# Optimization experiments

Hardware: AMD Instinct MI355X
Metric: run time of the kernel (lower is better)

## Reference

```python
import jax, jax.numpy as jnp
import numpy as np

D_MODEL = 512
D_STATE = 64
N_LAYERS = 6
L_SEQ = 784
BATCH = 64


def _layernorm(x, g, b, eps=1e-5):
    mu = x.mean(-1, keepdims=True)
    var = ((x - mu) ** 2).mean(-1, keepdims=True)
    return (x - mu) * jax.lax.rsqrt(var + eps) * g + b


def _s4d_kernel(log_dt, log_A_real, A_imag, C_re, C_im, L):
    # log_dt: (H,), others: (H, N). Returns real conv kernel (H, L).
    dt = jnp.exp(log_dt)[:, None]                      # (H,1)
    A = -jnp.exp(log_A_real) + 1j * A_imag             # (H,N) complex
    C = C_re + 1j * C_im                               # (H,N)
    dtA = A * dt                                       # (H,N)
    Cd = C * (jnp.exp(dtA) - 1.0) / A                  # ZOH-discretized C
    # Vandermonde: V[h,n,l] = exp(dtA[h,n] * l)
    V = jnp.exp(dtA[:, :, None] * jnp.arange(L, dtype=jnp.float32))  # (H,N,L)
    K = 2.0 * jnp.einsum('hn,hnl->hl', Cd, V).real     # (H,L)
    return K


def _s4_fftconv(u, K, D):
    # u: (B,L,H), K: (H,L), D: (H,)
    L = u.shape[1]
    uf = jnp.fft.rfft(u, 2 * L, axis=1)                # (B, L+1, H)
    kf = jnp.fft.rfft(K.T, 2 * L, axis=0)              # (L+1, H)
    y = jnp.fft.irfft(uf * kf[None], 2 * L, axis=1)[:, :L]
    return y + u * D


def setup_inputs() -> dict:
    key = jax.random.key(0)
    ks = jax.random.split(key, 12)
    H, N, NL = D_MODEL, D_STATE, N_LAYERS
    x = jax.random.normal(ks[0], (BATCH, L_SEQ, 1), dtype=jnp.float32)
    enc_w = jax.random.normal(ks[1], (1, H), dtype=jnp.float32) * 0.5
    enc_b = jnp.zeros((H,), dtype=jnp.float32)
    # S4D-Lin style init, stacked over layers
    log_dt = jnp.tile(
        jax.random.uniform(ks[2], (H,), minval=np.log(0.001), maxval=np.log(0.1)),
        (NL, 1))                                        # (NL,H)
    log_A_real = jnp.full((NL, H, N), jnp.log(0.5), dtype=jnp.float32)
    A_imag = jnp.tile(np.pi * jnp.arange(N, dtype=jnp.float32), (NL, H, 1))
    C_re = jax.random.normal(ks[3], (NL, H, N), dtype=jnp.float32) * (0.5 ** 0.5)
    C_im = jax.random.normal(ks[4], (NL, H, N), dtype=jnp.float32) * (0.5 ** 0.5)
    D = jax.random.normal(ks[5], (NL, H), dtype=jnp.float32)
    ln_g = jnp.ones((NL, H), dtype=jnp.float32)
    ln_b = jnp.zeros((NL, H), dtype=jnp.float32)
    fn_g = jnp.ones((H,), dtype=jnp.float32)
    fn_b = jnp.zeros((H,), dtype=jnp.float32)
    dec_w = jax.random.normal(ks[6], (H, 10), dtype=jnp.float32) / jnp.sqrt(H)
    dec_b = jnp.zeros((10,), dtype=jnp.float32)
    return dict(x=x, enc_w=enc_w, enc_b=enc_b, log_dt=log_dt,
                log_A_real=log_A_real, A_imag=A_imag, C_re=C_re, C_im=C_im,
                D=D, ln_g=ln_g, ln_b=ln_b, fn_g=fn_g, fn_b=fn_b,
                dec_w=dec_w, dec_b=dec_b)


def reference(x, enc_w, enc_b, log_dt, log_A_real, A_imag, C_re, C_im, D,
              ln_g, ln_b, fn_g, fn_b, dec_w, dec_b):
    h = x @ enc_w + enc_b                               # (B,L,H)
    L = h.shape[1]
    for i in range(log_dt.shape[0]):                    # fixed n_layers
        K = _s4d_kernel(log_dt[i], log_A_real[i], A_imag[i], C_re[i], C_im[i], L)
        z = _s4_fftconv(h, K, D[i])                     # S4 output (dropout=eval)
        h = _layernorm(h + z, ln_g[i], ln_b[i])         # residual + LN
    h = _layernorm(h, fn_g, fn_b)
    h = h.mean(axis=1)                                  # mean pool over seq
    return h @ dec_w + dec_b                            # (B,10)
```

## Files before the change

### kernel.cpp

```cpp
#include <hip/hip_runtime.h>
#include <hip/hip_bf16.h>

#define HD 512
#define NST 64
#define NLAY 6
#define LSEQ 784
#define BB 64
#define NKA 848
#define TOFF 800
#define LPADROWS 800
#define KSTR 850
#define CHK2 5
#define NCH 5
#define UTS2 9

typedef unsigned short u16;
typedef short s8v __attribute__((ext_vector_type(8)));
typedef float f16v __attribute__((ext_vector_type(16)));
typedef u16  u4h __attribute__((ext_vector_type(4)));
typedef u16  u8h __attribute__((ext_vector_type(8)));

__device__ __forceinline__ unsigned f2b(float f)
{
    unsigned u = __builtin_bit_cast(unsigned, f);
    return (u + 0x7FFFu + ((u >> 16) & 1u)) >> 16;
}
__device__ __forceinline__ float b2f16(u16 v)
{
    unsigned u = ((unsigned)v) << 16;
    return __builtin_bit_cast(float, u);
}

__global__ void precompute_k(const float* __restrict__ log_dt,
                             const float* __restrict__ log_A_real,
                             const float* __restrict__ A_imag,
                             const float* __restrict__ C_re,
                             const float* __restrict__ C_im,
                             float* __restrict__ lamr, float* __restrict__ lami,
                             float* __restrict__ dtr,  float* __restrict__ dti,
                             float* __restrict__ c2r,  float* __restrict__ c2i)
{
    int t = blockIdx.x * 256 + threadIdx.x;
    if (t >= NLAY * HD * NST) return;
    int ih = t >> 6;
    float dt  = expf(log_dt[ih]);
    float are = -expf(log_A_real[t]);
    float aim = A_imag[t];
    float dr = are * dt, di = aim * dt;
    float er = expf(dr);
    float sn, cs; __sincosf(di, &sn, &cs);
    float lr = er * cs, li = er * sn;
    float e1r = lr - 1.0f, e1i = li;
    float den = are * are + aim * aim;
    float qr = (e1r * are + e1i * aim) / den;
    float qi = (e1i * are - e1r * aim) / den;
    float crv = C_re[t], civ = C_im[t];
    lamr[t] = lr; lami[t] = li; dtr[t] = dr; dti[t] = di;
    c2r[t] = 2.0f * (crv * qr - civ * qi);
    c2i[t] = 2.0f * (crv * qi + civ * qr);
}

__global__ void kq_k(const float* __restrict__ lamr, const float* __restrict__ lami,
                     const float* __restrict__ dtr,  const float* __restrict__ dti,
                     const float* __restrict__ c2r,  const float* __restrict__ c2i,
                     u16* __restrict__ KA)
{
    int t = blockIdx.x * 256 + threadIdx.x;
    int dc = t % 49;
    int ih = t / 49;
    int d0 = dc * 16;
    float acc[16];
#pragma unroll
    for (int k = 0; k < 16; k++) acc[k] = 0.f;
    int base = ih * 64;
    for (int n = 0; n < 64; n++) {
        float lr = lamr[base + n], li = lami[base + n];
        float dr = dtr[base + n],  di = dti[base + n];
        float cr = c2r[base + n],  ci = c2i[base + n];
        float e = __expf(dr * (float)d0);
        float sn, cs; __sincosf(di * (float)d0, &sn, &cs);
        float pr = e * cs, pi = e * sn;
#pragma unroll
        for (int k = 0; k < 16; k++) {
            acc[k] = fmaf(cr, pr, fmaf(-ci, pi, acc[k]));
            float nr = pr * lr - pi * li;
            pi = fmaf(pr, li, pi * lr);
            pr = nr;
        }
    }
    u16* kap = KA + (size_t)ih * NKA;
#pragma unroll
    for (int k = 0; k < 16; k++)
        kap[TOFF - (d0 + k)] = (u16)f2b(acc[k]);
    if (dc == 0)  for (int z = TOFF + 1; z < NKA; z++) kap[z] = 0;
    if (dc == 48) for (int z = 0; z < TOFF - 783; z++) kap[z] = 0;
}

__global__ void xt_k(const float* __restrict__ x, float* __restrict__ xT)
{
    int t = blockIdx.x * 256 + threadIdx.x;
    int l = t >> 6, b = t & 63;
    xT[t] = x[b * LSEQ + l];
}

__global__ void encoder_k(const float* __restrict__ xT, const float* __restrict__ ew,
                          const float* __restrict__ eb, u16* __restrict__ Vb)
{
    int g = blockIdx.x * 256 + threadIdx.x;
    int bo = g & 7;
    int h  = (g >> 3) & 511;
    int l  = g >> 12;
    const float4* xp = (const float4*)&xT[l * BB + 8 * bo];
    float4 a0 = xp[0], a1 = xp[1];
    float w = ew[h], bb = eb[h];
    unsigned p0 = f2b(fmaf(a0.x, w, bb)) | (f2b(fmaf(a0.y, w, bb)) << 16);
    unsigned p1 = f2b(fmaf(a0.z, w, bb)) | (f2b(fmaf(a0.w, w, bb)) << 16);
    unsigned p2 = f2b(fmaf(a1.x, w, bb)) | (f2b(fmaf(a1.y, w, bb)) << 16);
    unsigned p3 = f2b(fmaf(a1.z, w, bb)) | (f2b(fmaf(a1.w, w, bb)) << 16);
    *(uint4*)&Vb[((size_t)l * HD + h) * BB + 8 * bo] = (uint4){p0, p1, p2, p3};
}

__global__ __launch_bounds__(128, 4)
void conv_k(const u16* __restrict__ Vb, u16* __restrict__ V2,
            const u16* __restrict__ KA, const float* __restrict__ Dvec)
{
    __shared__ __align__(16) u16 KR[6816];
    __shared__ __align__(16) unsigned UT[2][64 * UTS2];

    const int thr = threadIdx.x;
    const int h   = blockIdx.x & 511;
    const int c   = blockIdx.x >> 9;
    const int w   = thr >> 6;
    const int lane = thr & 63;
    const int n2 = lane & 31;
    const int qp = lane >> 5;
    const int JTN = 10 * c + 10;

    const u16* kap = KA + (size_t)h * NKA;
    {
        int s = thr & 7, ch = thr >> 3;
        int i0 = ch * 53;
        int i1 = (i0 + 53 < NKA) ? (i0 + 53) : NKA;
        u16* kr = KR + KSTR * s + ((8 - s) & 7);
        for (int i = i0; i < i1; i++) kr[i] = kap[i];
    }

    const int jj = thr >> 4;
    const int bq = thr & 15;
    {
        const u16* p = &Vb[((size_t)(2 * jj) * HD + h) * BB + 4 * bq];
        u4h r0 = *(const u4h*)p;
        u4h r1 = *(const u4h*)(p + (size_t)HD * BB);
        unsigned* up = &UT[0][0];
#pragma unroll
        for (int i = 0; i < 4; i++)
            up[(4 * bq + i) * UTS2 + jj] = (unsigned)r0[i] | ((unsigned)r1[i] << 16);
    }
    __syncthreads();

    f16v acc[CHK2];
#pragma unroll
    for (int i = 0; i < CHK2; i++)
#pragma unroll
        for (int r = 0; r < 16; r++) acc[i][r] = 0.f;

    const float dcoef = 1.0f + Dvec[h];

    const int s = lane & 7;
    const u16* krb = KR + KSTR * s + ((8 - s) & 7)
                     + (TOFF - 160 * c) + 8 * qp - n2;
    const unsigned* bb0 = &UT[0][(32 * w + n2) * UTS2 + 4 * qp];
    const unsigned* bb1 = &UT[1][(32 * w + n2) * UTS2 + 4 * qp];

    for (int jt = 0; jt < JTN; ++jt) {
        u4h r0, r1;
        const bool more = (jt + 1) < JTN;
        if (more) {
            int j = 16 * (jt + 1) + 2 * jj;
            const u16* p = &Vb[((size_t)j * HD + h) * BB + 4 * bq];
            r0 = *(const u4h*)p;
            r1 = *(const u4h*)(p + (size_t)HD * BB);
        }
        const unsigned* bb = (jt & 1) ? bb1 : bb0;
        union { unsigned u[4]; s8v v; } bu;
        bu.u[0] = bb[0]; bu.u[1] = bb[1]; bu.u[2] = bb[2]; bu.u[3] = bb[3];

        const u16* ap0 = krb + 16 * jt;
#pragma unroll
        for (int lt = 0; lt < CHK2; ++lt) {
            if (jt > 10 * c + 2 * lt + 1) continue;
            s8v av = *(const s8v*)__builtin_assume_aligned(ap0 - 32 * lt, 16);
            acc[lt] = __builtin_amdgcn_mfma_f32_32x32x16_bf16(av, bu.v, acc[lt], 0, 0, 0);
        }
        if (more) {
            unsigned* up = &UT[(jt & 1) ^ 1][0];
#pragma unroll
            for (int i = 0; i < 4; i++)
                up[(4 * bq + i) * UTS2 + jj] = (unsigned)r0[i] | ((unsigned)r1[i] << 16);
        }
        __syncthreads();
    }

#pragma unroll
    for (int lt = 0; lt < CHK2; ++lt) {
        const int l0 = 32 * (5 * c + lt) + 4 * qp;
#pragma unroll
        for (int r = 0; r < 16; ++r) {
            int l = l0 + (r & 3) + 8 * (r >> 2);
            size_t a = ((size_t)l * HD + h) * BB + 32 * w + n2;
            V2[a] = (u16)f2b(fmaf(dcoef, b2f16(Vb[a]), acc[lt][r]));
        }
    }
}

__global__ __launch_bounds__(512)
void lnT_k(const u16* __restrict__ src, u16* __restrict__ dst,
           const float* __restrict__ gp, const float* __restrict__ bp)
{
    __shared__ float redS[64][65], redQ[64][65];
    __shared__ float mus[64], rss[64];
    __shared__ float gs[512], bs[512];
    const int thr = threadIdx.x;
    const int bo = thr & 7;
    const int hg = thr >> 3;
    const size_t l = blockIdx.x;
    gs[thr] = gp[thr]; bs[thr] = bp[thr];

    const u16* sp = &src[(l * HD + hg * 8) * BB + 8 * bo];
    float v[64];
    float s[8] = {0, 0, 0, 0, 0, 0, 0, 0};
    float q[8] = {0, 0, 0, 0, 0, 0, 0, 0};
#pragma unroll
    for (int k = 0; k < 8; k++) {
        u8h r = *(const u8h*)(sp + (size_t)k * BB);
#pragma unroll
        for (int i = 0; i < 8; i++) {
            float x = b2f16(r[i]);
            v[k * 8 + i] = x;
            s[i] += x;
            q[i] = fmaf(x, x, q[i]);
        }
    }
#pragma unroll
    for (int i = 0; i < 8; i++) { redS[hg][8 * bo + i] = s[i]; redQ[hg][8 * bo + i] = q[i]; }
    __syncthreads();
    if (thr < 64) {
        float ts = 0.f, tq = 0.f;
#pragma unroll
        for (int g = 0; g < 64; g++) { ts += redS[g][thr]; tq += redQ[g][thr]; }
        float mu = ts * (1.0f / HD);
        mus[thr] = mu;
        rss[thr] = rsqrtf(tq * (1.0f / HD) - mu * mu + 1e-5f);
    }
    __syncthreads();
    float mu[8], rs[8];
#pragma unroll
    for (int i = 0; i < 8; i++) { mu[i] = mus[8 * bo + i]; rs[i] = rss[8 * bo + i]; }
    u16* dp = &dst[(l * HD + hg * 8) * BB + 8 * bo];
#pragma unroll
    for (int k = 0; k < 8; k++) {
        float g = gs[hg * 8 + k], bb = bs[hg * 8 + k];
        u8h w;
#pragma unroll
        for (int i = 0; i < 8; i++)
            w[i] = (u16)f2b(fmaf((v[k * 8 + i] - mu[i]) * rs[i], g, bb));
        *(u8h*)(dp + (size_t)k * BB) = w;
    }
}

__global__ void pool_k(const u16* __restrict__ Vb, float* __restrict__ PO)
{
    __shared__ float red[4][64];
    int h = blockIdx.x;
    int b = threadIdx.x & 63;
    int lg = threadIdx.x >> 6;
    const u16* p = &Vb[(size_t)h * BB + b];
    float s = 0.f;
    for (int l = lg; l < LSEQ; l += 4) s += b2f16(p[(size_t)l * HD * BB]);
    red[lg][b] = s;
    __syncthreads();
    if (threadIdx.x < 64) {
        float t = red[0][b] + red[1][b] + red[2][b] + red[3][b];
        PO[h * BB + b] = t * (1.0f / LSEQ);
    }
}

__global__ void dec_k(const float* __restrict__ PO, const float* __restrict__ w,
                      const float* __restrict__ bias, float* __restrict__ out)
{
    int t = blockIdx.x * 256 + threadIdx.x;
    if (t >= BB * 10) return;
    int cc = t % 10, b = t / 10;
    float acc = bias[cc];
    for (int hh = 0; hh < HD; hh++)
        acc = fmaf(PO[hh * BB + b], w[hh * 10 + cc], acc);
    out[t] = acc;
}

extern "C" void kernel_launch(void* const* d_in, const int* in_sizes, int n_in,
                              void* d_out, int out_size, void* d_ws, size_t ws_size,
                              hipStream_t stream)
{
    const float* x   = (const float*)d_in[0];
    const float* ew  = (const float*)d_in[1];
    const float* eb  = (const float*)d_in[2];
    const float* ldt = (const float*)d_in[3];
    const float* lar = (const float*)d_in[4];
    const float* aim = (const float*)d_in[5];
    const float* cre = (const float*)d_in[6];
    const float* cim = (const float*)d_in[7];
    const float* Dp  = (const float*)d_in[8];
    const float* lng = (const float*)d_in[9];
    const float* lnb = (const float*)d_in[10];
    const float* fng = (const float*)d_in[11];
    const float* fnb = (const float*)d_in[12];
    const float* dw  = (const float*)d_in[13];
    const float* db  = (const float*)d_in[14];
    float* out = (float*)d_out;

    const size_t SZ  = (size_t)BB * LSEQ * HD;
    const size_t SZB = (size_t)BB * LPADROWS * HD;
    const size_t PP  = (size_t)NLAY * HD * NST;
    u16*   Vb  = (u16*)d_ws;
    u16*   V2  = Vb + SZB;
    float* PAR = (float*)(V2 + SZB);
    float* lamr = PAR,        * lami = PAR + PP;
    float* dtr  = PAR + 2*PP, * dti  = PAR + 3*PP;
    float* c2r  = PAR + 4*PP, * c2i  = PAR + 5*PP;
    u16* KA = (u16*)(PAR + 6 * PP);
    float* PO = PAR + 6 * PP + (NLAY * HD * NKA) / 2;
    float* xT = PO + BB * HD;

    precompute_k<<<(NLAY * HD * NST + 255) / 256, 256, 0, stream>>>(
        ldt, lar, aim, cre, cim, lamr, lami, dtr, dti, c2r, c2i);
    kq_k<<<(NLAY * HD * 49) / 256, 256, 0, stream>>>(
        lamr, lami, dtr, dti, c2r, c2i, KA);
    xt_k<<<(LSEQ * BB) / 256, 256, 0, stream>>>(x, xT);
    encoder_k<<<(LSEQ * HD * 8) / 256, 256, 0, stream>>>(xT, ew, eb, Vb);

    for (int i = 0; i < NLAY; i++) {
        conv_k<<<512 * NCH, 128, 0, stream>>>(
            Vb, V2, KA + (size_t)i * HD * NKA, Dp + i * HD);
        lnT_k<<<LSEQ, 512, 0, stream>>>(V2, Vb, lng + i * HD, lnb + i * HD);
    }
    lnT_k<<<LSEQ, 512, 0, stream>>>(Vb, Vb, fng, fnb);
    pool_k<<<HD, 256, 0, stream>>>(Vb, PO);
    dec_k<<<(BB * 10 + 255) / 256, 256, 0, stream>>>(PO, dw, db, out);
}
```

Measured before the change: 631.6 us.

## Fuse layernorm apply into next conv input load, keep only stats pass

The per-layer layernorm kernel that read and rewrote the whole activation tensor is replaced. A lightweight stats kernel now writes only per-(l,b) mean and rstd. The next layer's conv applies the normalization while staging inputs into shared memory and in its residual/D term, and buffers ping-pong between layers. The last layer's LN is folded into the final LN kernel, and the block index mapping is reordered so that neighbouring blocks share the same channel. This removes one full-tensor write and read per layer, at the cost of extra stats loads and FMAs inside the conv loop.

```diff
diff --git a/kernel.cpp b/kernel.cpp
--- a/kernel.cpp
+++ b/kernel.cpp
@@ -120,21 +120,66 @@
     *(uint4*)&Vb[((size_t)l * HD + h) * BB + 8 * bo] = (uint4){p0, p1, p2, p3};
 }
 
+__global__ __launch_bounds__(256)
+void stats_k(const u16* __restrict__ P, float2* __restrict__ M)
+{
+    __shared__ float redS[32][65], redQ[32][65];
+    const int thr = threadIdx.x;
+    const size_t l = blockIdx.x;
+    if (l >= LSEQ) {
+        if (thr < BB) M[l * BB + thr] = make_float2(0.f, 1.f);
+        return;
+    }
+    const int bo = thr & 7;
+    const int ho = thr >> 3;
+    const u16* sp = &P[(l * HD + (size_t)ho * 16) * BB + 8 * bo];
+    float s[8] = {0, 0, 0, 0, 0, 0, 0, 0};
+    float q[8] = {0, 0, 0, 0, 0, 0, 0, 0};
+#pragma unroll
+    for (int k = 0; k < 16; k++) {
+        u8h r = *(const u8h*)(sp + (size_t)k * BB);
+#pragma unroll
+        for (int i = 0; i < 8; i++) {
+            float x = b2f16(r[i]);
+            s[i] += x;
+            q[i] = fmaf(x, x, q[i]);
+        }
+    }
+#pragma unroll
+    for (int i = 0; i < 8; i++) { redS[ho][8 * bo + i] = s[i]; redQ[ho][8 * bo + i] = q[i]; }
+    __syncthreads();
+    if (thr < 64) {
+        float ts = 0.f, tq = 0.f;
+#pragma unroll
+        for (int g = 0; g < 32; g++) { ts += redS[g][thr]; tq += redQ[g][thr]; }
+        float mu = ts * (1.0f / HD);
+        float rs = rsqrtf(tq * (1.0f / HD) - mu * mu + 1e-5f);
+        M[l * BB + thr] = make_float2(mu, rs);
+    }
+}
+
+template<int FLN>
 __global__ __launch_bounds__(128, 4)
 void conv_k(const u16* __restrict__ Vb, u16* __restrict__ V2,
-            const u16* __restrict__ KA, const float* __restrict__ Dvec)
+            const u16* __restrict__ KA, const float* __restrict__ Dvec,
+            const float2* __restrict__ M,
+            const float* __restrict__ gp, const float* __restrict__ bp)
 {
     __shared__ __align__(16) u16 KR[6816];
     __shared__ __align__(16) unsigned UT[2][64 * UTS2];
 
     const int thr = threadIdx.x;
-    const int h   = blockIdx.x & 511;
-    const int c   = blockIdx.x >> 9;
+    const int bid = blockIdx.x;
+    const int c   = bid % NCH;
+    const int h   = bid / NCH;
     const int w   = thr >> 6;
     const int lane = thr & 63;
     const int n2 = lane & 31;
     const int qp = lane >> 5;
     const int JTN = 10 * c + 10;
+
+    const float gh = FLN ? gp[h] : 0.f;
+    const float bh = FLN ? bp[h] : 0.f;
 
     const u16* kap = KA + (size_t)h * NKA;
     {
@@ -148,13 +193,30 @@
     const int jj = thr >> 4;
     const int bq = thr & 15;
     {
-        const u16* p = &Vb[((size_t)(2 * jj) * HD + h) * BB + 4 * bq];
+        const int j = 2 * jj;
+        const u16* p = &Vb[((size_t)j * HD + h) * BB + 4 * bq];
         u4h r0 = *(const u4h*)p;
         u4h r1 = *(const u4h*)(p + (size_t)HD * BB);
         unsigned* up = &UT[0][0];
-#pragma unroll
-        for (int i = 0; i < 4; i++)
-            up[(4 * bq + i) * UTS2 + jj] = (unsigned)r0[i] | ((unsigned)r1[i] << 16);
+        if (FLN) {
+            const float4* m0p = (const float4*)&M[(size_t)j * BB + 4 * bq];
+            const float4* m1p = (const float4*)&M[(size_t)(j + 1) * BB + 4 * bq];
+            float4 a0 = m0p[0], a1 = m0p[1], b0 = m1p[0], b1 = m1p[1];
+            float mu0[4] = {a0.x, a0.z, a1.x, a1.z};
+            float rs0[4] = {a0.y, a0.w, a1.y, a1.w};
+            float mu1[4] = {b0.x, b0.z, b1.x, b1.z};
+            float rs1[4] = {b0.y, b0.w, b1.y, b1.w};
+#pragma unroll
+            for (int i = 0; i < 4; i++) {
+                float x0 = fmaf(b2f16(r0[i]) - mu0[i], rs0[i] * gh, bh);
+                float x1 = fmaf(b2f16(r1[i]) - mu1[i], rs1[i] * gh, bh);
+                up[(4 * bq + i) * UTS2 + jj] = f2b(x0) | (f2b(x1) << 16);
+            }
+        } else {
+#pragma unroll
+            for (int i = 0; i < 4; i++)
+                up[(4 * bq + i) * UTS2 + jj] = (unsigned)r0[i] | ((unsigned)r1[i] << 16);
+        }
     }
     __syncthreads();
 
@@ -174,12 +236,18 @@
 
     for (int jt = 0; jt < JTN; ++jt) {
         u4h r0, r1;
+        float4 mA0, mB0, mA1, mB1;
         const bool more = (jt + 1) < JTN;
         if (more) {
             int j = 16 * (jt + 1) + 2 * jj;
             const u16* p = &Vb[((size_t)j * HD + h) * BB + 4 * bq];
             r0 = *(const u4h*)p;
             r1 = *(const u4h*)(p + (size_t)HD * BB);
+            if (FLN) {
+                const float4* m0p = (const float4*)&M[(size_t)j * BB + 4 * bq];
+                const float4* m1p = (const float4*)&M[(size_t)(j + 1) * BB + 4 * bq];
+                mA0 = m0p[0]; mB0 = m0p[1]; mA1 = m1p[0]; mB1 = m1p[1];
+            }
         }
         const unsigned* bb = (jt & 1) ? bb1 : bb0;
         union { unsigned u[4]; s8v v; } bu;
@@ -194,9 +262,22 @@
         }
         if (more) {
             unsigned* up = &UT[(jt & 1) ^ 1][0];
-#pragma unroll
-            for (int i = 0; i < 4; i++)
-                up[(4 * bq + i) * UTS2 + jj] = (unsigned)r0[i] | ((unsigned)r1[i] << 16);
+            if (FLN) {
+                float mu0[4] = {mA0.x, mA0.z, mB0.x, mB0.z};
+                float rs0[4] = {mA0.y, mA0.w, mB0.y, mB0.w};
+                float mu1[4] = {mA1.x, mA1.z, mB1.x, mB1.z};
+                float rs1[4] = {mA1.y, mA1.w, mB1.y, mB1.w};
+#pragma unroll
+                for (int i = 0; i < 4; i++) {
+                    float x0 = fmaf(b2f16(r0[i]) - mu0[i], rs0[i] * gh, bh);
+                    float x1 = fmaf(b2f16(r1[i]) - mu1[i], rs1[i] * gh, bh);
+                    up[(4 * bq + i) * UTS2 + jj] = f2b(x0) | (f2b(x1) << 16);
+                }
+            } else {
+#pragma unroll
+                for (int i = 0; i < 4; i++)
+                    up[(4 * bq + i) * UTS2 + jj] = (unsigned)r0[i] | ((unsigned)r1[i] << 16);
+            }
         }
         __syncthreads();
     }
@@ -208,14 +289,22 @@
         for (int r = 0; r < 16; ++r) {
             int l = l0 + (r & 3) + 8 * (r >> 2);
             size_t a = ((size_t)l * HD + h) * BB + 32 * w + n2;
-            V2[a] = (u16)f2b(fmaf(dcoef, b2f16(Vb[a]), acc[lt][r]));
+            float x = b2f16(Vb[a]);
+            float u = x;
+            if (FLN) {
+                float2 m = M[(size_t)l * BB + 32 * w + n2];
+                u = fmaf(x - m.x, m.y * gh, bh);
+            }
+            V2[a] = (u16)f2b(fmaf(dcoef, u, acc[lt][r]));
         }
     }
 }
 
 __global__ __launch_bounds__(512)
-void lnT_k(const u16* __restrict__ src, u16* __restrict__ dst,
-           const float* __restrict__ gp, const float* __restrict__ bp)
+void lnT2_k(const u16* __restrict__ src, u16* __restrict__ dst,
+            const float2* __restrict__ M,
+            const float* __restrict__ g5p, const float* __restrict__ b5p,
+            const float* __restrict__ gp, const float* __restrict__ bp)
 {
     __shared__ float redS[64][65], redQ[64][65];
     __shared__ float mus[64], rss[64];
@@ -226,16 +315,22 @@
     const size_t l = blockIdx.x;
     gs[thr] = gp[thr]; bs[thr] = bp[thr];
 
-    const u16* sp = &src[(l * HD + hg * 8) * BB + 8 * bo];
+    const float4* mp = (const float4*)&M[l * BB + 8 * bo];
+    float4 m0 = mp[0], m1 = mp[1], m2 = mp[2], m3 = mp[3];
+    float mu5[8] = {m0.x, m0.z, m1.x, m1.z, m2.x, m2.z, m3.x, m3.z};
+    float rs5[8] = {m0.y, m0.w, m1.y, m1.w, m2.y, m2.w, m3.y, m3.w};
+
+    const u16* sp = &src[(l * HD + (size_t)hg * 8) * BB + 8 * bo];
     float v[64];
     float s[8] = {0, 0, 0, 0, 0, 0, 0, 0};
     float q[8] = {0, 0, 0, 0, 0, 0, 0, 0};
 #pragma unroll
     for (int k = 0; k < 8; k++) {
         u8h r = *(const u8h*)(sp + (size_t)k * BB);
+        float g5 = g5p[hg * 8 + k], b5 = b5p[hg * 8 + k];
 #pragma unroll
         for (int i = 0; i < 8; i++) {
-            float x = b2f16(r[i]);
+            float x = fmaf(b2f16(r[i]) - mu5[i], rs5[i] * g5, b5);
             v[k * 8 + i] = x;
             s[i] += x;
             q[i] = fmaf(x, x, q[i]);
@@ -256,15 +351,15 @@
     float mu[8], rs[8];
 #pragma unroll
     for (int i = 0; i < 8; i++) { mu[i] = mus[8 * bo + i]; rs[i] = rss[8 * bo + i]; }
-    u16* dp = &dst[(l * HD + hg * 8) * BB + 8 * bo];
+    u16* dp = &dst[(l * HD + (size_t)hg * 8) * BB + 8 * bo];
 #pragma unroll
     for (int k = 0; k < 8; k++) {
         float g = gs[hg * 8 + k], bb = bs[hg * 8 + k];
-        u8h w;
+        u8h wv;
 #pragma unroll
         for (int i = 0; i < 8; i++)
-            w[i] = (u16)f2b(fmaf((v[k * 8 + i] - mu[i]) * rs[i], g, bb));
-        *(u8h*)(dp + (size_t)k * BB) = w;
+            wv[i] = (u16)f2b(fmaf((v[k * 8 + i] - mu[i]) * rs[i], g, bb));
+        *(u8h*)(dp + (size_t)k * BB) = wv;
     }
 }
 
@@ -318,7 +413,6 @@
     const float* db  = (const float*)d_in[14];
     float* out = (float*)d_out;
 
-    const size_t SZ  = (size_t)BB * LSEQ * HD;
     const size_t SZB = (size_t)BB * LPADROWS * HD;
     const size_t PP  = (size_t)NLAY * HD * NST;
     u16*   Vb  = (u16*)d_ws;
@@ -330,6 +424,7 @@
     u16* KA = (u16*)(PAR + 6 * PP);
     float* PO = PAR + 6 * PP + (NLAY * HD * NKA) / 2;
     float* xT = PO + BB * HD;
+    float2* M = (float2*)PAR;
 
     precompute_k<<<(NLAY * HD * NST + 255) / 256, 256, 0, stream>>>(
         ldt, lar, aim, cre, cim, lamr, lami, dtr, dti, c2r, c2i);
@@ -338,12 +433,17 @@
     xt_k<<<(LSEQ * BB) / 256, 256, 0, stream>>>(x, xT);
     encoder_k<<<(LSEQ * HD * 8) / 256, 256, 0, stream>>>(xT, ew, eb, Vb);
 
-    for (int i = 0; i < NLAY; i++) {
-        conv_k<<<512 * NCH, 128, 0, stream>>>(
-            Vb, V2, KA + (size_t)i * HD * NKA, Dp + i * HD);
-        lnT_k<<<LSEQ, 512, 0, stream>>>(V2, Vb, lng + i * HD, lnb + i * HD);
-    }
-    lnT_k<<<LSEQ, 512, 0, stream>>>(Vb, Vb, fng, fnb);
+    conv_k<0><<<512 * NCH, 128, 0, stream>>>(Vb, V2, KA, Dp, M, lng, lnb);
+    stats_k<<<LPADROWS, 256, 0, stream>>>(V2, M);
+    for (int i = 1; i < NLAY; i++) {
+        const u16* srcb = (i & 1) ? V2 : Vb;
+        u16*       dstb = (i & 1) ? Vb : V2;
+        conv_k<1><<<512 * NCH, 128, 0, stream>>>(
+            srcb, dstb, KA + (size_t)i * HD * NKA, Dp + i * HD,
+            M, lng + (size_t)(i - 1) * HD, lnb + (size_t)(i - 1) * HD);
+        stats_k<<<LPADROWS, 256, 0, stream>>>(dstb, M);
+    }
+    lnT2_k<<<LSEQ, 512, 0, stream>>>(Vb, Vb, M, lng + 5 * HD, lnb + 5 * HD, fng, fnb);
     pool_k<<<HD, 256, 0, stream>>>(Vb, PO);
     dec_k<<<(BB * 10 + 255) / 256, 256, 0, stream>>>(PO, dw, db, out);
 }
```

New measurement: 755.8 us. +19.7%, slower.
